# Kernel tuning notes

Hardware: AMD Instinct MI355X
Metric: run time of the kernel (lower is better)

## Reference

```python
import jax, jax.numpy as jnp
import numpy as np

VOCAB = 50257
EMB = 512


def setup_inputs() -> dict:
    key = jax.random.key(0)
    k1, k2, k3 = jax.random.split(key, 3)
    input_token_ids = jax.random.randint(k1, (8, 4096), 0, VOCAB, dtype=jnp.int64 if jax.config.jax_enable_x64 else jnp.int32)
    W = jax.random.normal(k2, (EMB, VOCAB), dtype=jnp.float32)  # nn.Linear(vocab, emb).weight
    b = jax.random.normal(k3, (EMB,), dtype=jnp.float32)        # nn.Linear bias
    return {"input_token_ids": input_token_ids, "W": W, "b": b}


def reference(input_token_ids, W, b):
    # one_hot(ids, V) @ W.T + b  ==  W.T[ids] + b   (exact same math, gather form)
    scale = jnp.asarray(EMB, W.dtype) ** 0.5
    emb = jnp.take(W.T, input_token_ids, axis=0)  # [B, S, EMB]
    return (emb + b) * scale
```

## Files before the change

kernel.cpp:

```cpp
#include <hip/hip_runtime.h>


constexpr int VOCAB = 50257;
constexpr int EMB   = 512;
constexpr int NTOK  = 8 * 4096;
constexpr float SCALE = 22.62741699796952f;

constexpr int VB  = 64;
constexpr int NB  = (VOCAB + VB - 1) / VB;
constexpr int CAP = 96;
constexpr int ECH = 64;
constexpr int NCH = EMB / ECH;
constexpr int RS  = VB + 1;


__global__ __launch_bounds__(256) void build_buckets(
    const int* __restrict__ ids,
    int* __restrict__ counts,
    int* __restrict__ olist,
    int* __restrict__ buckets)
{
    int t = blockIdx.x * 256 + threadIdx.x;
    int id = ids[t];
    int bkt = id >> 6;
    int slot = atomicAdd(&counts[bkt], 1);
    if (slot < CAP) {
        buckets[bkt * CAP + slot] = (t << 6) | (id & 63);
    } else {
        int o = atomicAdd(&counts[NB], 1);
        olist[o] = t;
    }
}

__global__ __launch_bounds__(256, 4) void scatter_main(
    const float* __restrict__ W,
    const float* __restrict__ bias,
    const int*   __restrict__ counts,
    const int*   __restrict__ buckets,
    float*       __restrict__ out)
{
    __shared__ float buf[2][ECH * RS];
    __shared__ int   toks[CAP];
    __shared__ int   s_cnt;

    const int b    = blockIdx.x;
    const int tid  = threadIdx.x;
    const int lane = tid & 63;
    const int w    = tid >> 6;

    if (tid == 0) s_cnt = counts[b];
    if (tid < CAP) toks[tid] = buckets[b * CAP + tid];

    float bb[NCH];
    #pragma unroll
    for (int c = 0; c < NCH; ++c) bb[c] = bias[c * ECH + lane];

    int v = b * VB + lane;
    const float* wsrc = W + (v < VOCAB ? v : VOCAB - 1);

    __syncthreads();
    const int cnt = min(s_cnt, CAP);
    if (cnt == 0) return;

    auto stage = [&](int c, int sel) {
        #pragma unroll
        for (int p = 0; p < 16; ++p) {
            const int rr = w * 16 + p;
            const float* gp = wsrc + (size_t)(c * ECH + rr) * VOCAB;
            float* lp = &buf[sel][rr * RS];
            __builtin_amdgcn_global_load_lds(
                (const __attribute__((address_space(1))) void*)gp,
                (__attribute__((address_space(3))) void*)lp, 4, 0, 0);
        }
    };

    stage(0, 0);

    #pragma unroll
    for (int c = 0; c < NCH; ++c) {
        const int sel = c & 1;
        if (c + 1 < NCH) {
            stage(c + 1, sel ^ 1);
            asm volatile("s_waitcnt vmcnt(16)" ::: "memory");
        } else {
            asm volatile("s_waitcnt vmcnt(0)" ::: "memory");
        }
        __builtin_amdgcn_s_barrier();

        const float  bc    = bb[c];
        const float* tilec = &buf[sel][lane * RS];
        float*       orow  = out + c * ECH + lane;
        for (int i = w; i < cnt; i += 4) {
            const int pk = toks[i];
            const int t  = pk >> 6;
            const int vl = pk & 63;
            __builtin_nontemporal_store((tilec[vl] + bc) * SCALE,
                                        orow + (size_t)t * EMB);
        }
        if (c + 1 < NCH) __builtin_amdgcn_s_barrier();
    }
}

__global__ __launch_bounds__(256) void overflow_fix(
    const int*   __restrict__ counts,
    const int*   __restrict__ olist,
    const int*   __restrict__ ids,
    const float* __restrict__ W,
    const float* __restrict__ bias,
    float*       __restrict__ out)
{
    int n    = counts[NB];
    int wid  = (blockIdx.x * 256 + threadIdx.x) >> 6;
    int lane = threadIdx.x & 63;
    int nw   = (gridDim.x * 256) >> 6;
    for (int ww = wid; ww < n; ww += nw) {
        int t  = olist[ww];
        int id = ids[t];
        #pragma unroll
        for (int m = 0; m < 8; ++m) {
            int e = lane + m * 64;
            out[(size_t)t * EMB + e] = (W[(size_t)e * VOCAB + id] + bias[e]) * SCALE;
        }
    }
}

__global__ __launch_bounds__(256) void embed_gather(
    const int*   __restrict__ ids,
    const float* __restrict__ W,
    const float* __restrict__ b,
    float*       __restrict__ out)
{
    int idx4 = blockIdx.x * blockDim.x + threadIdx.x;
    int t    = idx4 >> 7;
    int e    = (idx4 & 127) << 2;
    int id = ids[t];
    float4 bb = *reinterpret_cast<const float4*>(b + e);
    const float* wcol = W + (size_t)id;
    float4 o;
    o.x = (wcol[(size_t)(e + 0) * VOCAB] + bb.x) * SCALE;
    o.y = (wcol[(size_t)(e + 1) * VOCAB] + bb.y) * SCALE;
    o.z = (wcol[(size_t)(e + 2) * VOCAB] + bb.z) * SCALE;
    o.w = (wcol[(size_t)(e + 3) * VOCAB] + bb.w) * SCALE;
    *reinterpret_cast<float4*>(out + (size_t)idx4 * 4) = o;
}

extern "C" void kernel_launch(void* const* d_in, const int* in_sizes, int n_in,
                              void* d_out, int out_size, void* d_ws, size_t ws_size,
                              hipStream_t stream)
{
    const int*   ids  = (const int*)  d_in[0];
    const float* W    = (const float*)d_in[1];
    const float* bias = (const float*)d_in[2];
    float*       out  = (float*)d_out;

    const size_t ws_ints_needed = (size_t)NB + 1 + NTOK + (size_t)NB * CAP;

    if (ws_size >= ws_ints_needed * sizeof(int)) {
        int* counts  = (int*)d_ws;
        int* olist   = counts + NB + 1;
        int* buckets = olist + NTOK;

        hipMemsetAsync(counts, 0, (NB + 1) * sizeof(int), stream);
        build_buckets<<<NTOK / 256, 256, 0, stream>>>(ids, counts, olist, buckets);
        scatter_main<<<NB, 256, 0, stream>>>(W, bias, counts, buckets, out);
        overflow_fix<<<32, 256, 0, stream>>>(counts, olist, ids, W, bias, out);
    } else {
        constexpr int total4 = NTOK * EMB / 4;
        embed_gather<<<total4 / 256, 256, 0, stream>>>(ids, W, bias, out);
    }
}
```

Baseline: 199.9 us.

## Split scatter blocks across embedding quarters and fold overflow handling into main kernel

Each vocab bucket is now processed by four blocks, each covering 128 embedding rows, with every wave loading its own 32-row tile in one shot instead of a double-buffered 8-chunk pipeline with block barriers. The store loop now has each wave write two tokens per iteration as 32-float row segments, and the nontemporal store hint is dropped. The separate overflow kernel is merged into block-group 0, removing one launch. The aim is more parallelism and fewer barriers and launches, at the cost of less load/store overlap within a block and shorter contiguous stores.

```diff
diff --git a/kernel.cpp b/kernel.cpp
--- a/kernel.cpp
+++ b/kernel.cpp
@@ -6,12 +6,12 @@
 constexpr int NTOK  = 8 * 4096;
 constexpr float SCALE = 22.62741699796952f;
 
-constexpr int VB  = 64;
-constexpr int NB  = (VOCAB + VB - 1) / VB;
-constexpr int CAP = 96;
-constexpr int ECH = 64;
-constexpr int NCH = EMB / ECH;
-constexpr int RS  = VB + 1;
+constexpr int VB   = 64;
+constexpr int NB   = (VOCAB + VB - 1) / VB;
+constexpr int CAP  = 96;
+constexpr int ESPL = 4;
+constexpr int RWV  = 32;
+constexpr int RS   = VB + 1;
 
 
 __global__ __launch_bounds__(256) void build_buckets(
@@ -32,94 +32,72 @@
     }
 }
 
-__global__ __launch_bounds__(256, 4) void scatter_main(
+__global__ __launch_bounds__(256) void scatter_main(
     const float* __restrict__ W,
     const float* __restrict__ bias,
     const int*   __restrict__ counts,
     const int*   __restrict__ buckets,
+    const int*   __restrict__ olist,
+    const int*   __restrict__ ids,
     float*       __restrict__ out)
 {
-    __shared__ float buf[2][ECH * RS];
+    __shared__ float tile[4][RWV * RS];
     __shared__ int   toks[CAP];
     __shared__ int   s_cnt;
 
-    const int b    = blockIdx.x;
+    const int bid  = blockIdx.x;
+    const int b    = bid >> 2;
+    const int z    = bid & 3;
     const int tid  = threadIdx.x;
     const int lane = tid & 63;
     const int w    = tid >> 6;
 
     if (tid == 0) s_cnt = counts[b];
     if (tid < CAP) toks[tid] = buckets[b * CAP + tid];
+    __syncthreads();
+    const int cnt = min(s_cnt, CAP);
 
-    float bb[NCH];
-    #pragma unroll
-    for (int c = 0; c < NCH; ++c) bb[c] = bias[c * ECH + lane];
+    const int e0 = z * 128 + w * RWV;
+    const int el = lane & 31;
+    const float be = bias[e0 + el];
 
-    int v = b * VB + lane;
+    const int v = b * VB + lane;
     const float* wsrc = W + (v < VOCAB ? v : VOCAB - 1);
 
-    __syncthreads();
-    const int cnt = min(s_cnt, CAP);
-    if (cnt == 0) return;
-
-    auto stage = [&](int c, int sel) {
+    if (cnt > 0) {
         #pragma unroll
-        for (int p = 0; p < 16; ++p) {
-            const int rr = w * 16 + p;
-            const float* gp = wsrc + (size_t)(c * ECH + rr) * VOCAB;
-            float* lp = &buf[sel][rr * RS];
+        for (int r = 0; r < RWV; ++r) {
+            const float* gp = wsrc + (size_t)(e0 + r) * VOCAB;
+            float* lp = &tile[w][r * RS];
             __builtin_amdgcn_global_load_lds(
                 (const __attribute__((address_space(1))) void*)gp,
                 (__attribute__((address_space(3))) void*)lp, 4, 0, 0);
         }
-    };
+        asm volatile("s_waitcnt vmcnt(0)" ::: "memory");
 
-    stage(0, 0);
+        const int half = lane >> 5;
+        const float* tw = &tile[w][el * RS];
+        for (int i = 0; i < cnt; i += 2) {
+            int j  = i + half;
+            int jj = j < cnt ? j : cnt - 1;
+            int pk = toks[jj];
+            int t  = pk >> 6;
+            int vl = pk & 63;
+            float val = (tw[vl] + be) * SCALE;
+            if (j < cnt) out[(size_t)t * EMB + e0 + el] = val;
+        }
+    }
 
-    #pragma unroll
-    for (int c = 0; c < NCH; ++c) {
-        const int sel = c & 1;
-        if (c + 1 < NCH) {
-            stage(c + 1, sel ^ 1);
-            asm volatile("s_waitcnt vmcnt(16)" ::: "memory");
-        } else {
-            asm volatile("s_waitcnt vmcnt(0)" ::: "memory");
-        }
-        __builtin_amdgcn_s_barrier();
-
-        const float  bc    = bb[c];
-        const float* tilec = &buf[sel][lane * RS];
-        float*       orow  = out + c * ECH + lane;
-        for (int i = w; i < cnt; i += 4) {
-            const int pk = toks[i];
-            const int t  = pk >> 6;
-            const int vl = pk & 63;
-            __builtin_nontemporal_store((tilec[vl] + bc) * SCALE,
-                                        orow + (size_t)t * EMB);
-        }
-        if (c + 1 < NCH) __builtin_amdgcn_s_barrier();
-    }
-}
-
-__global__ __launch_bounds__(256) void overflow_fix(
-    const int*   __restrict__ counts,
-    const int*   __restrict__ olist,
-    const int*   __restrict__ ids,
-    const float* __restrict__ W,
-    const float* __restrict__ bias,
-    float*       __restrict__ out)
-{
-    int n    = counts[NB];
-    int wid  = (blockIdx.x * 256 + threadIdx.x) >> 6;
-    int lane = threadIdx.x & 63;
-    int nw   = (gridDim.x * 256) >> 6;
-    for (int ww = wid; ww < n; ww += nw) {
-        int t  = olist[ww];
-        int id = ids[t];
-        #pragma unroll
-        for (int m = 0; m < 8; ++m) {
-            int e = lane + m * 64;
-            out[(size_t)t * EMB + e] = (W[(size_t)e * VOCAB + id] + bias[e]) * SCALE;
+    if (b == 0) {
+        int n = counts[NB];
+        for (int ww = w; ww < n; ww += 4) {
+            int t  = olist[ww];
+            int id = ids[t];
+            #pragma unroll
+            for (int m = 0; m < 2; ++m) {
+                int e = z * 128 + lane + m * 64;
+                out[(size_t)t * EMB + e] = (W[(size_t)e * VOCAB + id] + bias[e]) * SCALE;
+            }
         }
     }
 }
@@ -162,8 +140,8 @@
 
         hipMemsetAsync(counts, 0, (NB + 1) * sizeof(int), stream);
         build_buckets<<<NTOK / 256, 256, 0, stream>>>(ids, counts, olist, buckets);
-        scatter_main<<<NB, 256, 0, stream>>>(W, bias, counts, buckets, out);
-        overflow_fix<<<32, 256, 0, stream>>>(counts, olist, ids, W, bias, out);
+        scatter_main<<<NB * ESPL, 256, 0, stream>>>(W, bias, counts, buckets,
+                                                    olist, ids, out);
     } else {
         constexpr int total4 = NTOK * EMB / 4;
         embed_gather<<<total4 / 256, 256, 0, stream>>>(ids, W, bias, out);
```

Measured after the change: 195.9 us. 2.0% less time.
